# Performance work log

Measured on AMD Instinct MI355X. Metric: run time of the kernel, lower is better.

Reference implementation:

```python
import jax, jax.numpy as jnp
import numpy as np


def setup_inputs() -> dict:
    key = jax.random.key(0)
    kL, kx = jax.random.split(key)
    N, D, K = 4096, 256, 8
    L = jax.random.normal(kL, (N, N), dtype=jnp.float32)
    x = jax.random.normal(kx, (N, D), dtype=jnp.float32)
    # Taylor-like decaying filter coefficients (fixed, non-trained in the original)
    coeffs = jnp.asarray([1.0, 0.9, 0.45, 0.15, 0.0375, 0.0075, 0.00125, 0.000179],
                         dtype=jnp.float32)
    return {"L": L, "x": x, "coeffs": coeffs}


def reference(L, x, coeffs):
    """filter = sum_i coeffs[i] * L^i ; out = filter @ x.

    Same math as torch.stack([c*L.matrix_power(i)]).sum(0) @ x, but the powers
    are built with a single running product instead of K independent
    matrix_power calls.
    """
    N = L.shape[0]
    K = coeffs.shape[0]
    P = jnp.eye(N, dtype=L.dtype)          # L^0
    filt = coeffs[0] * P
    for i in range(1, K):                   # small fixed polynomial order
        P = P @ L                            # L^i
        filt = filt + coeffs[i] * P
    return filt @ x                          # [N, D]
```

## Files before the change

kernel.cpp:

```cpp
#include <hip/hip_runtime.h>
#include <hip/hip_bf16.h>

#define NDIM 4096
#define DDIM 256
#define KORD 8

#define BM 128
#define BN 128
#define BK 32
#define SPLITK 8
#define KSLICE (NDIM / SPLITK)
#define NSTEP (KSLICE / BK)
#define ELEMS (NDIM * DDIM)

#define LBUF 16384

typedef __attribute__((ext_vector_type(8))) short bf16x8;
typedef __attribute__((ext_vector_type(4))) float f32x4;

__device__ __forceinline__ ushort f2bf(float v) {
    __hip_bfloat16 h = __float2bfloat16(v);
    return *reinterpret_cast<ushort*>(&h);
}
__device__ __forceinline__ float bf2f(ushort u) {
    __hip_bfloat16 h = *reinterpret_cast<__hip_bfloat16*>(&u);
    return __bfloat162float(h);
}
__device__ __forceinline__ void split2(float v, ushort& h, ushort& l) {
    h = f2bf(v);
    l = f2bf(v - bf2f(h));
}
__device__ __forceinline__ uint4 pack8(const ushort* s) {
    uint4 r;
    r.x = (uint)s[0] | ((uint)s[1] << 16);
    r.y = (uint)s[2] | ((uint)s[3] << 16);
    r.z = (uint)s[4] | ((uint)s[5] << 16);
    r.w = (uint)s[6] | ((uint)s[7] << 16);
    return r;
}

__global__ __launch_bounds__(256)
void split_L(const float* __restrict__ L, ushort* __restrict__ Lhi,
             ushort* __restrict__ Llo)
{
    const int e0 = (blockIdx.x * 256 + threadIdx.x) * 8;
    float4 a = *(const float4*)&L[e0];
    float4 b = *(const float4*)&L[e0 + 4];
    float v[8] = {a.x, a.y, a.z, a.w, b.x, b.y, b.z, b.w};
    ushort h[8], l[8];
#pragma unroll
    for (int j = 0; j < 8; ++j) split2(v[j], h[j], l[j]);
    *(uint4*)&Lhi[e0] = pack8(h);
    *(uint4*)&Llo[e0] = pack8(l);
}

__global__ __launch_bounds__(256)
void split_x(const float* __restrict__ x, const float* __restrict__ coeffs,
             ushort* __restrict__ yhiT, ushort* __restrict__ yloT)
{
    __shared__ float tile[64][65];
    const float c = coeffs[KORD - 1];
    const int m0 = blockIdx.x * 64, n0 = blockIdx.y * 64;
    const int t = threadIdx.x;
    const int ml = t >> 2, n4 = (t & 3) * 16;
#pragma unroll
    for (int j = 0; j < 4; ++j) {
        float4 v = *(const float4*)&x[(size_t)(m0 + ml) * DDIM + n0 + n4 + j * 4];
        tile[ml][n4 + j * 4 + 0] = c * v.x;
        tile[ml][n4 + j * 4 + 1] = c * v.y;
        tile[ml][n4 + j * 4 + 2] = c * v.z;
        tile[ml][n4 + j * 4 + 3] = c * v.w;
    }
    __syncthreads();
    const int nl = t >> 2, m16 = (t & 3) * 16;
    ushort h[16], l[16];
#pragma unroll
    for (int j = 0; j < 16; ++j) split2(tile[m16 + j][nl], h[j], l[j]);
    const size_t ob = (size_t)(n0 + nl) * NDIM + m0 + m16;
    *(uint4*)&yhiT[ob]     = pack8(h);
    *(uint4*)&yhiT[ob + 8] = pack8(h + 8);
    *(uint4*)&yloT[ob]     = pack8(l);
    *(uint4*)&yloT[ob + 8] = pack8(l + 8);
}

__global__ __launch_bounds__(256)
void gemm_fused(const ushort* __restrict__ Lhi, const ushort* __restrict__ Llo,
                const ushort* __restrict__ yhiT, const ushort* __restrict__ yloT,
                float* __restrict__ P)
{
    __shared__ ushort lds[2 * LBUF];

    const int bid  = blockIdx.x;
    const int z    = bid & 7;
    const int slot = bid >> 3;
    const int nt   = slot & 1;
    const int mt   = slot >> 1;

    const int m0 = mt * BM, n0 = nt * BN;
    const int kb = z * KSLICE;

    const int t = threadIdx.x;
    const int lane = t & 63, wid = t >> 6;
    const int wr = wid >> 1, wc = wid & 1;

    const int rowS = t >> 2;
    const int ksw  = ((t & 3) ^ ((t >> 3) & 3)) * 8;
    const ushort* sAh = Lhi  + (size_t)(m0 + rowS) * NDIM + kb + ksw;
    const ushort* sAl = Llo  + (size_t)(m0 + rowS) * NDIM + kb + ksw;
    const ushort* sBh = yhiT + (size_t)(n0 + rowS) * NDIM + kb + ksw;
    const ushort* sBl = yloT + (size_t)(n0 + rowS) * NDIM + kb + ksw;
    const size_t R64 = (size_t)64 * NDIM;
    const int wb = wid * 512;

#define GLD(src, dstoff)                                                     \
    __builtin_amdgcn_global_load_lds(                                        \
        (const __attribute__((address_space(1))) uint*)(src),                \
        (__attribute__((address_space(3))) uint*)(&lds[dstoff]), 16, 0, 0)

#define STAGE(buf, ko)                                                       \
    do {                                                                     \
        const int _b = (buf) * LBUF;                                         \
        GLD(sAh + (ko),       _b + wb);                                      \
        GLD(sAh + (ko) + R64, _b + 2048 + wb);                               \
        GLD(sAl + (ko),       _b + 4096 + wb);                               \
        GLD(sAl + (ko) + R64, _b + 6144 + wb);                               \
        GLD(sBh + (ko),       _b + 8192 + wb);                               \
        GLD(sBh + (ko) + R64, _b + 10240 + wb);                              \
        GLD(sBl + (ko),       _b + 12288 + wb);                              \
        GLD(sBl + (ko) + R64, _b + 14336 + wb);                              \
    } while (0)

    const int frow = lane & 15;
    const int fsw  = ((lane >> 4) ^ ((frow >> 1) & 3)) * 8;
    const int arB  = (wr * 64 + frow) * 32 + fsw;
    const int brB  = 8192 + (wc * 64 + frow) * 32 + fsw;

    f32x4 acc[4][4];
#pragma unroll
    for (int i = 0; i < 4; ++i)
#pragma unroll
        for (int j = 0; j < 4; ++j) acc[i][j] = (f32x4){0.f, 0.f, 0.f, 0.f};

    STAGE(0, 0);
    STAGE(1, BK);

    for (int step = 0; step < NSTEP; ++step) {
        if (step + 1 < NSTEP)
            asm volatile("s_waitcnt vmcnt(8)" ::: "memory");
        else
            asm volatile("s_waitcnt vmcnt(0)" ::: "memory");
        __builtin_amdgcn_sched_barrier(0);
        __builtin_amdgcn_s_barrier();
        __builtin_amdgcn_sched_barrier(0);

        const int b = (step & 1) * LBUF;
        bf16x8 ah[4], al[4], bh[4], bl[4];
#pragma unroll
        for (int i = 0; i < 4; ++i) {
            ah[i] = *(const bf16x8*)&lds[b + arB + i * 512];
            al[i] = *(const bf16x8*)&lds[b + arB + i * 512 + 4096];
        }
#pragma unroll
        for (int j = 0; j < 4; ++j) {
            bh[j] = *(const bf16x8*)&lds[b + brB + j * 512];
            bl[j] = *(const bf16x8*)&lds[b + brB + j * 512 + 4096];
        }
        asm volatile("s_waitcnt lgkmcnt(0)" ::: "memory");
        __builtin_amdgcn_sched_barrier(0);
        __builtin_amdgcn_s_barrier();
        __builtin_amdgcn_sched_barrier(0);

        if (step + 2 < NSTEP) STAGE(step & 1, (step + 2) * BK);

        __builtin_amdgcn_s_setprio(1);
#pragma unroll
        for (int i = 0; i < 4; ++i)
#pragma unroll
            for (int j = 0; j < 4; ++j) {
                acc[i][j] = __builtin_amdgcn_mfma_f32_16x16x32_bf16(
                    ah[i], bh[j], acc[i][j], 0, 0, 0);
                acc[i][j] = __builtin_amdgcn_mfma_f32_16x16x32_bf16(
                    ah[i], bl[j], acc[i][j], 0, 0, 0);
                acc[i][j] = __builtin_amdgcn_mfma_f32_16x16x32_bf16(
                    al[i], bh[j], acc[i][j], 0, 0, 0);
            }
        __builtin_amdgcn_s_setprio(0);
    }
#undef STAGE
#undef GLD

    float* Pp = P + (size_t)z * ELEMS;
    const int crow = (lane >> 4) * 4;
    const int ccol = lane & 15;
#pragma unroll
    for (int i = 0; i < 4; ++i)
#pragma unroll
        for (int j = 0; j < 4; ++j)
#pragma unroll
            for (int r = 0; r < 4; ++r)
                Pp[(size_t)(m0 + wr * 64 + i * 16 + crow + r) * DDIM
                   + n0 + wc * 64 + j * 16 + ccol] = acc[i][j][r];
}

__global__ __launch_bounds__(256)
void combine(const float* __restrict__ P, const float* __restrict__ x,
             const float* __restrict__ coeffs, const int ci, const int last,
             ushort* __restrict__ yhiT, ushort* __restrict__ yloT,
             float* __restrict__ out)
{
    __shared__ float tile[64][65];
    const float c = coeffs[ci];
    const int m0 = blockIdx.x * 64, n0 = blockIdx.y * 64;
    const int t = threadIdx.x;
    const int ml = t >> 2, n4 = (t & 3) * 16;
    const size_t base = (size_t)(m0 + ml) * DDIM + n0 + n4;
    float acc[16];
#pragma unroll
    for (int j = 0; j < 4; ++j) {
        float4 v = *(const float4*)&x[base + j * 4];
        acc[j * 4 + 0] = c * v.x; acc[j * 4 + 1] = c * v.y;
        acc[j * 4 + 2] = c * v.z; acc[j * 4 + 3] = c * v.w;
    }
#pragma unroll
    for (int s = 0; s < SPLITK; ++s) {
        const float* Pp = P + (size_t)s * ELEMS;
#pragma unroll
        for (int j = 0; j < 4; ++j) {
            float4 v = *(const float4*)&Pp[base + j * 4];
            acc[j * 4 + 0] += v.x; acc[j * 4 + 1] += v.y;
            acc[j * 4 + 2] += v.z; acc[j * 4 + 3] += v.w;
        }
    }
    if (last) {
#pragma unroll
        for (int j = 0; j < 4; ++j) {
            float4 v;
            v.x = acc[j * 4 + 0]; v.y = acc[j * 4 + 1];
            v.z = acc[j * 4 + 2]; v.w = acc[j * 4 + 3];
            *(float4*)&out[base + j * 4] = v;
        }
        return;
    }
#pragma unroll
    for (int j = 0; j < 16; ++j) tile[ml][n4 + j] = acc[j];
    __syncthreads();
    const int nl = t >> 2, m16 = (t & 3) * 16;
    ushort h[16], l[16];
#pragma unroll
    for (int j = 0; j < 16; ++j) split2(tile[m16 + j][nl], h[j], l[j]);
    const size_t ob = (size_t)(n0 + nl) * NDIM + m0 + m16;
    *(uint4*)&yhiT[ob]     = pack8(h);
    *(uint4*)&yhiT[ob + 8] = pack8(h + 8);
    *(uint4*)&yloT[ob]     = pack8(l);
    *(uint4*)&yloT[ob + 8] = pack8(l + 8);
}

extern "C" void kernel_launch(void* const* d_in, const int* in_sizes, int n_in,
                              void* d_out, int out_size, void* d_ws, size_t ws_size,
                              hipStream_t stream)
{
    const float* L      = (const float*)d_in[0];
    const float* x      = (const float*)d_in[1];
    const float* coeffs = (const float*)d_in[2];
    float* out = (float*)d_out;

    char* w = (char*)d_ws;
    ushort* Lhi  = (ushort*)w;
    ushort* Llo  = (ushort*)(w + (size_t)NDIM * NDIM * 2);
    float*  Pp   = (float*)(w + (size_t)NDIM * NDIM * 4);
    ushort* yhiT = (ushort*)(w + (size_t)NDIM * NDIM * 4 + (size_t)SPLITK * ELEMS * 4);
    ushort* yloT = yhiT + (size_t)DDIM * NDIM;

    split_L<<<NDIM * NDIM / (256 * 8), 256, 0, stream>>>(L, Lhi, Llo);
    split_x<<<dim3(NDIM / 64, DDIM / 64), 256, 0, stream>>>(x, coeffs, yhiT, yloT);

    for (int i = KORD - 2; i >= 0; --i) {
        gemm_fused<<<SPLITK * 64, 256, 0, stream>>>(Lhi, Llo, yhiT, yloT, Pp);
        combine<<<dim3(NDIM / 64, DDIM / 64), 256, 0, stream>>>(
            Pp, x, coeffs, i, (i == 0) ? 1 : 0, yhiT, yloT, out);
    }
}
```

Measured before the change: 327.9 us.

## Split LDS staging into halves interleaved with MFMA compute phases

Splits each k-step's MFMA work into two column halves and issues the next tile's A-half global-to-LDS loads after the first half and B-half loads after the second. The aim is to overlap global loads with matrix math instead of doing all reads, then a barrier, then all loads. It drops the explicit lgkmcnt wait and the sched_barriers around the barriers and adds an extra barrier per step. The A half of the buffer is overwritten while B rows 2-3 are still read from the same buffer, which is safe because A and B sit in separate regions. Relying on compiler-inserted waits may still risk hazards.

```diff
diff --git a/kernel.cpp b/kernel.cpp
--- a/kernel.cpp
+++ b/kernel.cpp
@@ -117,13 +117,18 @@
         (const __attribute__((address_space(1))) uint*)(src),                \
         (__attribute__((address_space(3))) uint*)(&lds[dstoff]), 16, 0, 0)
 
-#define STAGE(buf, ko)                                                       \
+#define STAGE_HALF_A(buf, ko)                                                \
     do {                                                                     \
         const int _b = (buf) * LBUF;                                         \
         GLD(sAh + (ko),       _b + wb);                                      \
         GLD(sAh + (ko) + R64, _b + 2048 + wb);                               \
         GLD(sAl + (ko),       _b + 4096 + wb);                               \
         GLD(sAl + (ko) + R64, _b + 6144 + wb);                               \
+    } while (0)
+
+#define STAGE_HALF_B(buf, ko)                                                \
+    do {                                                                     \
+        const int _b = (buf) * LBUF;                                         \
         GLD(sBh + (ko),       _b + 8192 + wb);                               \
         GLD(sBh + (ko) + R64, _b + 10240 + wb);                              \
         GLD(sBl + (ko),       _b + 12288 + wb);                              \
@@ -141,52 +146,73 @@
 #pragma unroll
         for (int j = 0; j < 4; ++j) acc[i][j] = (f32x4){0.f, 0.f, 0.f, 0.f};
 
-    STAGE(0, 0);
-    STAGE(1, BK);
+    STAGE_HALF_A(0, 0);
+    STAGE_HALF_B(0, 0);
+    STAGE_HALF_A(1, BK);
+    STAGE_HALF_B(1, BK);
 
     for (int step = 0; step < NSTEP; ++step) {
         if (step + 1 < NSTEP)
             asm volatile("s_waitcnt vmcnt(8)" ::: "memory");
         else
             asm volatile("s_waitcnt vmcnt(0)" ::: "memory");
-        __builtin_amdgcn_sched_barrier(0);
         __builtin_amdgcn_s_barrier();
-        __builtin_amdgcn_sched_barrier(0);
 
         const int b = (step & 1) * LBUF;
-        bf16x8 ah[4], al[4], bh[4], bl[4];
+
+        bf16x8 ah[4], al[4], bh01[2], bl01[2];
 #pragma unroll
         for (int i = 0; i < 4; ++i) {
             ah[i] = *(const bf16x8*)&lds[b + arB + i * 512];
             al[i] = *(const bf16x8*)&lds[b + arB + i * 512 + 4096];
         }
 #pragma unroll
-        for (int j = 0; j < 4; ++j) {
-            bh[j] = *(const bf16x8*)&lds[b + brB + j * 512];
-            bl[j] = *(const bf16x8*)&lds[b + brB + j * 512 + 4096];
-        }
-        asm volatile("s_waitcnt lgkmcnt(0)" ::: "memory");
-        __builtin_amdgcn_sched_barrier(0);
-        __builtin_amdgcn_s_barrier();
-        __builtin_amdgcn_sched_barrier(0);
-
-        if (step + 2 < NSTEP) STAGE(step & 1, (step + 2) * BK);
-
+        for (int j = 0; j < 2; ++j) {
+            bh01[j] = *(const bf16x8*)&lds[b + brB + j * 512];
+            bl01[j] = *(const bf16x8*)&lds[b + brB + j * 512 + 4096];
+        }
         __builtin_amdgcn_s_setprio(1);
 #pragma unroll
         for (int i = 0; i < 4; ++i)
 #pragma unroll
-            for (int j = 0; j < 4; ++j) {
+            for (int j = 0; j < 2; ++j) {
                 acc[i][j] = __builtin_amdgcn_mfma_f32_16x16x32_bf16(
-                    ah[i], bh[j], acc[i][j], 0, 0, 0);
+                    ah[i], bh01[j], acc[i][j], 0, 0, 0);
                 acc[i][j] = __builtin_amdgcn_mfma_f32_16x16x32_bf16(
-                    ah[i], bl[j], acc[i][j], 0, 0, 0);
+                    ah[i], bl01[j], acc[i][j], 0, 0, 0);
                 acc[i][j] = __builtin_amdgcn_mfma_f32_16x16x32_bf16(
-                    al[i], bh[j], acc[i][j], 0, 0, 0);
+                    al[i], bh01[j], acc[i][j], 0, 0, 0);
             }
         __builtin_amdgcn_s_setprio(0);
-    }
-#undef STAGE
+        __builtin_amdgcn_s_barrier();
+
+        if (step + 2 < NSTEP) STAGE_HALF_A(step & 1, (step + 2) * BK);
+
+        bf16x8 bh23[2], bl23[2];
+#pragma unroll
+        for (int j = 0; j < 2; ++j) {
+            bh23[j] = *(const bf16x8*)&lds[b + brB + (j + 2) * 512];
+            bl23[j] = *(const bf16x8*)&lds[b + brB + (j + 2) * 512 + 4096];
+        }
+        __builtin_amdgcn_s_setprio(1);
+#pragma unroll
+        for (int i = 0; i < 4; ++i)
+#pragma unroll
+            for (int j = 0; j < 2; ++j) {
+                acc[i][j + 2] = __builtin_amdgcn_mfma_f32_16x16x32_bf16(
+                    ah[i], bh23[j], acc[i][j + 2], 0, 0, 0);
+                acc[i][j + 2] = __builtin_amdgcn_mfma_f32_16x16x32_bf16(
+                    ah[i], bl23[j], acc[i][j + 2], 0, 0, 0);
+                acc[i][j + 2] = __builtin_amdgcn_mfma_f32_16x16x32_bf16(
+                    al[i], bh23[j], acc[i][j + 2], 0, 0, 0);
+            }
+        __builtin_amdgcn_s_setprio(0);
+        __builtin_amdgcn_s_barrier();
+
+        if (step + 2 < NSTEP) STAGE_HALF_B(step & 1, (step + 2) * BK);
+    }
+#undef STAGE_HALF_A
+#undef STAGE_HALF_B
 #undef GLD
 
     float* Pp = P + (size_t)z * ELEMS;
```

Result: no change. 325.2 us (-0.8%).
